# Optimization experiments

Hardware: AMD Instinct MI355X
Metric: run time of the kernel (lower is better)

Reference implementation:

```python
import jax, jax.numpy as jnp
import numpy as np

TEMPERATURE = 2.0
SOFT_LAMBDA = 0.5
SMOOTH_L1_BETA = 1.0  # CFG.smooth_l1_beta (torch default)
EPS_COS = 1e-8
EPS_LOG = 1e-7


def _offdiag(x):
    # x: [n, n] -> [n, n-1], dropping the diagonal, preserving column order.
    n = x.shape[0]
    cols = jnp.arange(n - 1)
    idx = cols[None, :] + (cols[None, :] >= jnp.arange(n)[:, None])
    return x[jnp.arange(n)[:, None], idx]


def _cos_pair_diff(v):
    # 1 - pairwise cosine similarity, norms clamped at eps (torch CosineSimilarity).
    nv = jnp.maximum(jnp.linalg.norm(v, axis=-1), EPS_COS)
    cos = (v @ v.T) / (nv[:, None] * nv[None, :])
    return 1.0 - cos


def setup_inputs() -> dict:
    key = jax.random.key(0)
    k1, k2, k3, k4, k5 = jax.random.split(key, 5)
    n, d_feat = 384, 128
    return {
        "trans_feat": jax.random.normal(k1, (n, d_feat), dtype=jnp.float32),
        "rot_green": jax.random.normal(k2, (n, 3), dtype=jnp.float32),
        "rot_red": jax.random.normal(k3, (n, 3), dtype=jnp.float32),
        "trans": jax.random.normal(k4, (n, 3), dtype=jnp.float32),
        "sym": jax.random.randint(k5, (n, 1), 0, 2, dtype=jnp.int32),
    }


def reference(trans_feat, rot_green, rot_red, trans, sym):
    n = trans_feat.shape[0]

    # ---- label differences ----
    # trans: smooth-L1 over pairwise diffs, mean over coord dim -> [n, n]
    d = trans[:, None, :] - trans[None, :, :]
    ad = jnp.abs(d)
    sl1 = jnp.where(ad < SMOOTH_L1_BETA, 0.5 * d * d / SMOOTH_L1_BETA, ad - 0.5 * SMOOTH_L1_BETA)
    trans_diff = sl1.mean(-1)

    g = _cos_pair_diff(rot_green)
    r = _cos_pair_diff(rot_red)
    sym_mask = sym[:, 0] == 1
    pair_sym = sym_mask[:, None] | sym_mask[None, :]
    rot_diff = jnp.where(pair_sym, g, g + r)

    # ---- feature similarity logits (negative L2, zero-safe norm) ----
    fd = trans_feat[:, None, :] - trans_feat[None, :, :]
    sq = jnp.sum(fd * fd, axis=-1)
    norm = jnp.where(sq > 0, jnp.sqrt(jnp.where(sq > 0, sq, 1.0)), 0.0)
    logits = -norm / TEMPERATURE
    logits = logits - jnp.max(logits, axis=1, keepdims=True)
    exp_logits = jnp.exp(logits)

    lo = _offdiag(logits)      # [n, n-1]
    eo = _offdiag(exp_logits)  # [n, n-1]
    td = _offdiag(trans_diff)  # [n, n-1]
    rd = _offdiag(rot_diff)    # [n, n-1]

    # rank masks: mask[i, j, k] = diff[i, j] <= diff[i, k]
    trans_mask = td[:, :, None] <= td[:, None, :]
    hard_mask = trans_mask & (rd[:, :, None] <= rd[:, None, :])

    den_trans = jnp.einsum('ijk,ik->ij', trans_mask.astype(lo.dtype), eo)
    den_hard = jnp.einsum('ijk,ik->ij', hard_mask.astype(lo.dtype), eo)

    pos_trans = lo - jnp.log(den_trans + EPS_LOG)
    pos_hard = lo - jnp.log(den_hard + EPS_LOG)

    denom = n * (n - 1)
    loss_hard = -jnp.sum(pos_hard) / denom
    loss_trans = -jnp.sum(pos_trans) / denom
    return loss_hard + SOFT_LAMBDA * loss_trans
```

## Files before the change

### kernel.cpp

```cpp
#include <hip/hip_runtime.h>
#include <math.h>

#define N 384
#define DF 128
#define TI 16
#define TK 16
#define TEMP 2.0f
#define SOFT_LAMBDA 0.5f
#define BETA 1.0f
#define EPS_COS 1e-8f
#define EPS_LOG 1e-7f

__global__ __launch_bounds__(256) void rnc_pairs(
    const float* __restrict__ feat,
    const float* __restrict__ rg,
    const float* __restrict__ rr,
    const float* __restrict__ tr,
    const int*   __restrict__ sym,
    float4* __restrict__ pk)
{
    const int i0 = blockIdx.y * TI;
    const int k0 = blockIdx.x * TK;
    const int t = threadIdx.x;

    __shared__ __align__(16) float4 fi_s[TI][DF / 4 + 1];
    __shared__ __align__(16) float4 fk_s[TK][DF / 4 + 1];
    __shared__ float4 hi_s[TI], gi_s[TI], ri_s[TI];
    __shared__ float4 hk_s[TK], gk_s[TK], rk_s[TK];

    if (t < TI) {
        int g = i0 + t;
        hi_s[t] = make_float4(tr[g * 3], tr[g * 3 + 1], tr[g * 3 + 2],
                              (sym[g] == 1) ? 1.f : 0.f);
        float a = rg[g * 3], b = rg[g * 3 + 1], c = rg[g * 3 + 2];
        gi_s[t] = make_float4(a, b, c, fmaxf(sqrtf(a * a + b * b + c * c), EPS_COS));
        float d = rr[g * 3], e = rr[g * 3 + 1], f = rr[g * 3 + 2];
        ri_s[t] = make_float4(d, e, f, fmaxf(sqrtf(d * d + e * e + f * f), EPS_COS));
    } else if (t >= 32 && t < 32 + TK) {
        int g = k0 + (t - 32);
        int tl = t - 32;
        hk_s[tl] = make_float4(tr[g * 3], tr[g * 3 + 1], tr[g * 3 + 2],
                               (sym[g] == 1) ? 1.f : 0.f);
        float a = rg[g * 3], b = rg[g * 3 + 1], c = rg[g * 3 + 2];
        gk_s[tl] = make_float4(a, b, c, fmaxf(sqrtf(a * a + b * b + c * c), EPS_COS));
        float d = rr[g * 3], e = rr[g * 3 + 1], f = rr[g * 3 + 2];
        rk_s[tl] = make_float4(d, e, f, fmaxf(sqrtf(d * d + e * e + f * f), EPS_COS));
    }

    const float4* feat4 = reinterpret_cast<const float4*>(feat);
#pragma unroll
    for (int idx = 0; idx < 2; ++idx) {
        int u = t + idx * 256;
        int row = u >> 5, c = u & 31;
        fi_s[row][c] = feat4[(i0 + row) * (DF / 4) + c];
        fk_s[row][c] = feat4[(k0 + row) * (DF / 4) + c];
    }
    __syncthreads();

    const int ii = t >> 4, kk = t & 15;
    float sq = 0.f;
#pragma unroll
    for (int d = 0; d < DF / 4; ++d) {
        float4 a = fi_s[ii][d];
        float4 b = fk_s[kk][d];
        float dx = a.x - b.x, dy = a.y - b.y, dz = a.z - b.z, dw = a.w - b.w;
        sq += dx * dx + dy * dy + dz * dz + dw * dw;
    }
    const int gi = i0 + ii, gk = k0 + kk;
    float dist = (sq > 0.f) ? sqrtf(sq) : 0.f;
    float lo = -dist * (1.0f / TEMP);
    float eo = (gi == gk) ? 0.f : expf(lo);

    float4 ha = hi_s[ii], hb = hk_s[kk];
    float s = 0.f;
    {
        float d0 = ha.x - hb.x, d1 = ha.y - hb.y, d2 = ha.z - hb.z;
        float a0 = fabsf(d0), a1 = fabsf(d1), a2 = fabsf(d2);
        s += (a0 < BETA) ? (0.5f * d0 * d0 / BETA) : (a0 - 0.5f * BETA);
        s += (a1 < BETA) ? (0.5f * d1 * d1 / BETA) : (a1 - 0.5f * BETA);
        s += (a2 < BETA) ? (0.5f * d2 * d2 / BETA) : (a2 - 0.5f * BETA);
    }
    float td = s * (1.0f / 3.0f);

    float4 ga = gi_s[ii], gb = gk_s[kk];
    float gdiff = 1.0f - (ga.x * gb.x + ga.y * gb.y + ga.z * gb.z) / (ga.w * gb.w);
    float4 ra = ri_s[ii], rb = rk_s[kk];
    float rdiff = 1.0f - (ra.x * rb.x + ra.y * rb.y + ra.z * rb.z) / (ra.w * rb.w);
    bool pair_sym = (ha.w != 0.f) || (hb.w != 0.f);
    float rd = pair_sym ? gdiff : (gdiff + rdiff);

    pk[gi * N + gk] = make_float4(td, rd, eo, lo);
}

__global__ __launch_bounds__(512) void rnc_rank(
    const float4* __restrict__ pk,
    float* __restrict__ partial_h,
    float* __restrict__ partial_t)
{
    const int i = blockIdx.x >> 1;
    const int h = blockIdx.x & 1;
    const int t = threadIdx.x;

    __shared__ __align__(16) float4 pks[N];
    __shared__ __align__(16) float2 dp[192][8];
    __shared__ float red_h[8], red_t[8];

    if (t < N) pks[t] = pk[i * N + t];
    __syncthreads();

    const int w = t >> 6, l = t & 63;
    const int jl = l * 3;
    float tdj[3], rdj[3];
    float dent[3] = {0.f, 0.f, 0.f};
    float denh[3] = {0.f, 0.f, 0.f};
#pragma unroll
    for (int jj = 0; jj < 3; ++jj) {
        float4 p = pks[h * 192 + jl + jj];
        tdj[jj] = p.x;
        rdj[jj] = p.y;
    }
    const int k0 = w * 48;
#pragma unroll 4
    for (int k = k0; k < k0 + 48; ++k) {
        float4 p = pks[k];
#pragma unroll
        for (int jj = 0; jj < 3; ++jj) {
            bool mt = p.x >= tdj[jj];
            bool mh = mt && (p.y >= rdj[jj]);
            dent[jj] += mt ? p.z : 0.f;
            denh[jj] += mh ? p.z : 0.f;
        }
    }
#pragma unroll
    for (int jj = 0; jj < 3; ++jj) dp[jl + jj][w] = make_float2(dent[jj], denh[jj]);
    __syncthreads();

    float pos_h = 0.f, pos_t = 0.f;
    if (t < 192) {
        const int j = h * 192 + t;
        if (j != i) {
            float st_ = 0.f, sh_ = 0.f;
#pragma unroll
            for (int g = 0; g < 8; ++g) {
                float2 v = dp[t][g];
                st_ += v.x;
                sh_ += v.y;
            }
            float lo = pks[j].w;
            pos_h = lo - logf(sh_ + EPS_LOG);
            pos_t = lo - logf(st_ + EPS_LOG);
        }
    }
#pragma unroll
    for (int off = 32; off > 0; off >>= 1) {
        pos_h += __shfl_down(pos_h, off, 64);
        pos_t += __shfl_down(pos_t, off, 64);
    }
    if (l == 0) {
        red_h[w] = pos_h;
        red_t[w] = pos_t;
    }
    __syncthreads();
    if (t == 0) {
        float sh = 0.f, st = 0.f;
#pragma unroll
        for (int g = 0; g < 8; ++g) {
            sh += red_h[g];
            st += red_t[g];
        }
        partial_h[blockIdx.x] = sh;
        partial_t[blockIdx.x] = st;
    }
}

__global__ __launch_bounds__(768) void rnc_final(
    const float* __restrict__ partial_h,
    const float* __restrict__ partial_t,
    float* __restrict__ out)
{
    const int t = threadIdx.x;
    float hsum = partial_h[t];
    float tsum = partial_t[t];
#pragma unroll
    for (int off = 32; off > 0; off >>= 1) {
        hsum += __shfl_down(hsum, off, 64);
        tsum += __shfl_down(tsum, off, 64);
    }
    __shared__ float rh[12], rt[12];
    const int wave = t >> 6, lane = t & 63;
    if (lane == 0) {
        rh[wave] = hsum;
        rt[wave] = tsum;
    }
    __syncthreads();
    if (t == 0) {
        double sh = 0.0, st = 0.0;
#pragma unroll
        for (int w = 0; w < 12; ++w) {
            sh += (double)rh[w];
            st += (double)rt[w];
        }
        const double denom = (double)N * (double)(N - 1);
        out[0] = (float)(-(sh + (double)SOFT_LAMBDA * st) / denom);
    }
}

extern "C" void kernel_launch(void* const* d_in, const int* in_sizes, int n_in,
                              void* d_out, int out_size, void* d_ws, size_t ws_size,
                              hipStream_t stream) {
    const float* feat = (const float*)d_in[0];
    const float* rg   = (const float*)d_in[1];
    const float* rr   = (const float*)d_in[2];
    const float* tr   = (const float*)d_in[3];
    const int*   sym  = (const int*)d_in[4];
    float* out = (float*)d_out;

    float4* pk = (float4*)d_ws;
    float* partial_h = (float*)((char*)d_ws + (size_t)N * N * sizeof(float4));
    float* partial_t = partial_h + 2 * N;

    dim3 gridA(N / TK, N / TI);
    rnc_pairs<<<gridA, 256, 0, stream>>>(feat, rg, rr, tr, sym, pk);
    rnc_rank<<<2 * N, 512, 0, stream>>>(pk, partial_h, partial_t);
    rnc_final<<<1, 2 * N, 0, stream>>>(partial_h, partial_t, out);
}
```

Baseline: 79.81 us.

## Use norm-expansion dot products with 2x2 register tiles and atomic final reduce

The pairwise feature kernel now computes squared distances as |a|^2+|b|^2-2a·b, using 64-thread blocks where each thread produces a 2x2 tile of pairs so shared-memory loads are reused. The third reduction kernel is removed: the rank kernel atomically adds its scaled partial sums into the output, which the first kernel zeroes. This cuts one launch and reduces the LDS traffic per pair. In exchange it adds cancellation error in the distance and a nondeterministic float atomic summation order.

```diff
diff --git a/kernel.cpp b/kernel.cpp
--- a/kernel.cpp
+++ b/kernel.cpp
@@ -3,32 +3,41 @@
 
 #define N 384
 #define DF 128
-#define TI 16
-#define TK 16
 #define TEMP 2.0f
 #define SOFT_LAMBDA 0.5f
 #define BETA 1.0f
 #define EPS_COS 1e-8f
 #define EPS_LOG 1e-7f
 
-__global__ __launch_bounds__(256) void rnc_pairs(
+__global__ __launch_bounds__(64) void rnc_pairs(
     const float* __restrict__ feat,
     const float* __restrict__ rg,
     const float* __restrict__ rr,
     const float* __restrict__ tr,
     const int*   __restrict__ sym,
-    float4* __restrict__ pk)
+    float4* __restrict__ pk,
+    float* __restrict__ out)
 {
-    const int i0 = blockIdx.y * TI;
-    const int k0 = blockIdx.x * TK;
+    const int i0 = blockIdx.y * 16;
+    const int k0 = blockIdx.x * 16;
     const int t = threadIdx.x;
 
-    __shared__ __align__(16) float4 fi_s[TI][DF / 4 + 1];
-    __shared__ __align__(16) float4 fk_s[TK][DF / 4 + 1];
-    __shared__ float4 hi_s[TI], gi_s[TI], ri_s[TI];
-    __shared__ float4 hk_s[TK], gk_s[TK], rk_s[TK];
-
-    if (t < TI) {
+    __shared__ __align__(16) float4 fa[16][33];
+    __shared__ __align__(16) float4 fb[16][33];
+    __shared__ float nsq[2][16];
+    __shared__ float4 hi_s[16], gi_s[16], ri_s[16];
+    __shared__ float4 hk_s[16], gk_s[16], rk_s[16];
+
+    if (blockIdx.x == 0 && blockIdx.y == 0 && t == 0) out[0] = 0.f;
+
+    const float4* feat4 = reinterpret_cast<const float4*>(feat);
+#pragma unroll
+    for (int u = t; u < 512; u += 64) {
+        int row = u >> 5, c = u & 31;
+        fa[row][c] = feat4[(i0 + row) * (DF / 4) + c];
+        fb[row][c] = feat4[(k0 + row) * (DF / 4) + c];
+    }
+    if (t < 16) {
         int g = i0 + t;
         hi_s[t] = make_float4(tr[g * 3], tr[g * 3 + 1], tr[g * 3 + 2],
                               (sym[g] == 1) ? 1.f : 0.f);
@@ -36,9 +45,8 @@
         gi_s[t] = make_float4(a, b, c, fmaxf(sqrtf(a * a + b * b + c * c), EPS_COS));
         float d = rr[g * 3], e = rr[g * 3 + 1], f = rr[g * 3 + 2];
         ri_s[t] = make_float4(d, e, f, fmaxf(sqrtf(d * d + e * e + f * f), EPS_COS));
-    } else if (t >= 32 && t < 32 + TK) {
-        int g = k0 + (t - 32);
-        int tl = t - 32;
+    } else if (t < 32) {
+        int tl = t - 16, g = k0 + tl;
         hk_s[tl] = make_float4(tr[g * 3], tr[g * 3 + 1], tr[g * 3 + 2],
                                (sym[g] == 1) ? 1.f : 0.f);
         float a = rg[g * 3], b = rg[g * 3 + 1], c = rg[g * 3 + 2];
@@ -46,56 +54,70 @@
         float d = rr[g * 3], e = rr[g * 3 + 1], f = rr[g * 3 + 2];
         rk_s[tl] = make_float4(d, e, f, fmaxf(sqrtf(d * d + e * e + f * f), EPS_COS));
     }
-
-    const float4* feat4 = reinterpret_cast<const float4*>(feat);
-#pragma unroll
-    for (int idx = 0; idx < 2; ++idx) {
-        int u = t + idx * 256;
-        int row = u >> 5, c = u & 31;
-        fi_s[row][c] = feat4[(i0 + row) * (DF / 4) + c];
-        fk_s[row][c] = feat4[(k0 + row) * (DF / 4) + c];
-    }
-    __syncthreads();
-
-    const int ii = t >> 4, kk = t & 15;
-    float sq = 0.f;
-#pragma unroll
-    for (int d = 0; d < DF / 4; ++d) {
-        float4 a = fi_s[ii][d];
-        float4 b = fk_s[kk][d];
-        float dx = a.x - b.x, dy = a.y - b.y, dz = a.z - b.z, dw = a.w - b.w;
-        sq += dx * dx + dy * dy + dz * dz + dw * dw;
-    }
-    const int gi = i0 + ii, gk = k0 + kk;
-    float dist = (sq > 0.f) ? sqrtf(sq) : 0.f;
-    float lo = -dist * (1.0f / TEMP);
-    float eo = (gi == gk) ? 0.f : expf(lo);
-
-    float4 ha = hi_s[ii], hb = hk_s[kk];
-    float s = 0.f;
-    {
-        float d0 = ha.x - hb.x, d1 = ha.y - hb.y, d2 = ha.z - hb.z;
-        float a0 = fabsf(d0), a1 = fabsf(d1), a2 = fabsf(d2);
-        s += (a0 < BETA) ? (0.5f * d0 * d0 / BETA) : (a0 - 0.5f * BETA);
-        s += (a1 < BETA) ? (0.5f * d1 * d1 / BETA) : (a1 - 0.5f * BETA);
-        s += (a2 < BETA) ? (0.5f * d2 * d2 / BETA) : (a2 - 0.5f * BETA);
-    }
-    float td = s * (1.0f / 3.0f);
-
-    float4 ga = gi_s[ii], gb = gk_s[kk];
-    float gdiff = 1.0f - (ga.x * gb.x + ga.y * gb.y + ga.z * gb.z) / (ga.w * gb.w);
-    float4 ra = ri_s[ii], rb = rk_s[kk];
-    float rdiff = 1.0f - (ra.x * rb.x + ra.y * rb.y + ra.z * rb.z) / (ra.w * rb.w);
-    bool pair_sym = (ha.w != 0.f) || (hb.w != 0.f);
-    float rd = pair_sym ? gdiff : (gdiff + rdiff);
-
-    pk[gi * N + gk] = make_float4(td, rd, eo, lo);
+    __syncthreads();
+
+    if (t < 32) {
+        int which = t >> 4, r = t & 15;
+        float s = 0.f;
+#pragma unroll
+        for (int d4 = 0; d4 < DF / 4; ++d4) {
+            float4 v = which ? fb[r][d4] : fa[r][d4];
+            s += v.x * v.x + v.y * v.y + v.z * v.z + v.w * v.w;
+        }
+        nsq[which][r] = s;
+    }
+    __syncthreads();
+
+    const int tx = t & 7, ty = t >> 3;
+    const int ia = 2 * ty, ka = 2 * tx;
+    float d00 = 0.f, d01 = 0.f, d10 = 0.f, d11 = 0.f;
+#pragma unroll
+    for (int d4 = 0; d4 < DF / 4; ++d4) {
+        float4 a0 = fa[ia][d4];
+        float4 a1 = fa[ia + 1][d4];
+        float4 b0 = fb[ka][d4];
+        float4 b1 = fb[ka + 1][d4];
+        d00 += a0.x * b0.x + a0.y * b0.y + a0.z * b0.z + a0.w * b0.w;
+        d01 += a0.x * b1.x + a0.y * b1.y + a0.z * b1.z + a0.w * b1.w;
+        d10 += a1.x * b0.x + a1.y * b0.y + a1.z * b0.z + a1.w * b0.w;
+        d11 += a1.x * b1.x + a1.y * b1.y + a1.z * b1.z + a1.w * b1.w;
+    }
+    float dots[2][2] = {{d00, d01}, {d10, d11}};
+
+#pragma unroll
+    for (int ii = 0; ii < 2; ++ii) {
+#pragma unroll
+        for (int kk = 0; kk < 2; ++kk) {
+            const int li = ia + ii, lk = ka + kk;
+            const int gi = i0 + li, gk = k0 + lk;
+            float sq = nsq[0][li] + nsq[1][lk] - 2.f * dots[ii][kk];
+            float dist = (sq > 0.f) ? sqrtf(sq) : 0.f;
+            float lo = -dist * (1.0f / TEMP);
+            float eo = (gi == gk) ? 0.f : expf(lo);
+
+            float4 ha = hi_s[li], hb = hk_s[lk];
+            float d0 = ha.x - hb.x, d1 = ha.y - hb.y, d2 = ha.z - hb.z;
+            float a0 = fabsf(d0), a1 = fabsf(d1), a2 = fabsf(d2);
+            float s = ((a0 < BETA) ? (0.5f * d0 * d0 / BETA) : (a0 - 0.5f * BETA))
+                    + ((a1 < BETA) ? (0.5f * d1 * d1 / BETA) : (a1 - 0.5f * BETA))
+                    + ((a2 < BETA) ? (0.5f * d2 * d2 / BETA) : (a2 - 0.5f * BETA));
+            float td = s * (1.0f / 3.0f);
+
+            float4 ga = gi_s[li], gb = gk_s[lk];
+            float gdiff = 1.0f - (ga.x * gb.x + ga.y * gb.y + ga.z * gb.z) / (ga.w * gb.w);
+            float4 ra = ri_s[li], rb = rk_s[lk];
+            float rdiff = 1.0f - (ra.x * rb.x + ra.y * rb.y + ra.z * rb.z) / (ra.w * rb.w);
+            bool pair_sym = (ha.w != 0.f) || (hb.w != 0.f);
+            float rd = pair_sym ? gdiff : (gdiff + rdiff);
+
+            pk[gi * N + gk] = make_float4(td, rd, eo, lo);
+        }
+    }
 }
 
 __global__ __launch_bounds__(512) void rnc_rank(
     const float4* __restrict__ pk,
-    float* __restrict__ partial_h,
-    float* __restrict__ partial_t)
+    float* __restrict__ out)
 {
     const int i = blockIdx.x >> 1;
     const int h = blockIdx.x & 1;
@@ -168,40 +190,8 @@
             sh += red_h[g];
             st += red_t[g];
         }
-        partial_h[blockIdx.x] = sh;
-        partial_t[blockIdx.x] = st;
-    }
-}
-
-__global__ __launch_bounds__(768) void rnc_final(
-    const float* __restrict__ partial_h,
-    const float* __restrict__ partial_t,
-    float* __restrict__ out)
-{
-    const int t = threadIdx.x;
-    float hsum = partial_h[t];
-    float tsum = partial_t[t];
-#pragma unroll
-    for (int off = 32; off > 0; off >>= 1) {
-        hsum += __shfl_down(hsum, off, 64);
-        tsum += __shfl_down(tsum, off, 64);
-    }
-    __shared__ float rh[12], rt[12];
-    const int wave = t >> 6, lane = t & 63;
-    if (lane == 0) {
-        rh[wave] = hsum;
-        rt[wave] = tsum;
-    }
-    __syncthreads();
-    if (t == 0) {
-        double sh = 0.0, st = 0.0;
-#pragma unroll
-        for (int w = 0; w < 12; ++w) {
-            sh += (double)rh[w];
-            st += (double)rt[w];
-        }
-        const double denom = (double)N * (double)(N - 1);
-        out[0] = (float)(-(sh + (double)SOFT_LAMBDA * st) / denom);
+        const float scale = -1.0f / ((float)N * (float)(N - 1));
+        atomicAdd(out, (sh + SOFT_LAMBDA * st) * scale);
     }
 }
 
@@ -216,11 +206,8 @@
     float* out = (float*)d_out;
 
     float4* pk = (float4*)d_ws;
-    float* partial_h = (float*)((char*)d_ws + (size_t)N * N * sizeof(float4));
-    float* partial_t = partial_h + 2 * N;
-
-    dim3 gridA(N / TK, N / TI);
-    rnc_pairs<<<gridA, 256, 0, stream>>>(feat, rg, rr, tr, sym, pk);
-    rnc_rank<<<2 * N, 512, 0, stream>>>(pk, partial_h, partial_t);
-    rnc_final<<<1, 2 * N, 0, stream>>>(partial_h, partial_t, out);
+
+    dim3 gridA(N / 16, N / 16);
+    rnc_pairs<<<gridA, 64, 0, stream>>>(feat, rg, rr, tr, sym, pk, out);
+    rnc_rank<<<2 * N, 512, 0, stream>>>(pk, out);
 }
```

Result: slower. 84.58 us (+6.0%).

## Drop final reduction kernel via atomicAdd and process full rows per rank block

Applied to the files above, without the earlier changes.

The separate final-reduction launch is removed. The pairs kernel zeroes the output, and each rank block atomically adds its scaled partial sum into it. The rank kernel now handles a whole row i per block, six j per thread instead of three, which halves the block count and reloads each pk row once instead of twice. This saves one launch and the duplicated row loads, at the cost of more register pressure, fewer blocks for parallelism, and non-deterministic float atomic accumulation order.

```diff
diff --git a/kernel.cpp b/kernel.cpp
--- a/kernel.cpp
+++ b/kernel.cpp
@@ -17,7 +17,8 @@
     const float* __restrict__ rr,
     const float* __restrict__ tr,
     const int*   __restrict__ sym,
-    float4* __restrict__ pk)
+    float4* __restrict__ pk,
+    float* __restrict__ out)
 {
     const int i0 = blockIdx.y * TI;
     const int k0 = blockIdx.x * TK;
@@ -27,6 +28,8 @@
     __shared__ __align__(16) float4 fk_s[TK][DF / 4 + 1];
     __shared__ float4 hi_s[TI], gi_s[TI], ri_s[TI];
     __shared__ float4 hk_s[TK], gk_s[TK], rk_s[TK];
+
+    if (blockIdx.x == 0 && blockIdx.y == 0 && t == 0) out[0] = 0.f;
 
     if (t < TI) {
         int g = i0 + t;
@@ -72,14 +75,11 @@
     float eo = (gi == gk) ? 0.f : expf(lo);
 
     float4 ha = hi_s[ii], hb = hk_s[kk];
-    float s = 0.f;
-    {
-        float d0 = ha.x - hb.x, d1 = ha.y - hb.y, d2 = ha.z - hb.z;
-        float a0 = fabsf(d0), a1 = fabsf(d1), a2 = fabsf(d2);
-        s += (a0 < BETA) ? (0.5f * d0 * d0 / BETA) : (a0 - 0.5f * BETA);
-        s += (a1 < BETA) ? (0.5f * d1 * d1 / BETA) : (a1 - 0.5f * BETA);
-        s += (a2 < BETA) ? (0.5f * d2 * d2 / BETA) : (a2 - 0.5f * BETA);
-    }
+    float d0 = ha.x - hb.x, d1 = ha.y - hb.y, d2 = ha.z - hb.z;
+    float a0 = fabsf(d0), a1 = fabsf(d1), a2 = fabsf(d2);
+    float s = ((a0 < BETA) ? (0.5f * d0 * d0 / BETA) : (a0 - 0.5f * BETA))
+            + ((a1 < BETA) ? (0.5f * d1 * d1 / BETA) : (a1 - 0.5f * BETA))
+            + ((a2 < BETA) ? (0.5f * d2 * d2 / BETA) : (a2 - 0.5f * BETA));
     float td = s * (1.0f / 3.0f);
 
     float4 ga = gi_s[ii], gb = gk_s[kk];
@@ -94,28 +94,27 @@
 
 __global__ __launch_bounds__(512) void rnc_rank(
     const float4* __restrict__ pk,
-    float* __restrict__ partial_h,
-    float* __restrict__ partial_t)
+    float* __restrict__ out)
 {
-    const int i = blockIdx.x >> 1;
-    const int h = blockIdx.x & 1;
+    const int i = blockIdx.x;
     const int t = threadIdx.x;
 
     __shared__ __align__(16) float4 pks[N];
-    __shared__ __align__(16) float2 dp[192][8];
+    __shared__ float dpt[8][N];
+    __shared__ float dph[8][N];
     __shared__ float red_h[8], red_t[8];
 
     if (t < N) pks[t] = pk[i * N + t];
     __syncthreads();
 
     const int w = t >> 6, l = t & 63;
-    const int jl = l * 3;
-    float tdj[3], rdj[3];
-    float dent[3] = {0.f, 0.f, 0.f};
-    float denh[3] = {0.f, 0.f, 0.f};
+    const int jb = l * 6;
+    float tdj[6], rdj[6];
+    float dent[6] = {0.f, 0.f, 0.f, 0.f, 0.f, 0.f};
+    float denh[6] = {0.f, 0.f, 0.f, 0.f, 0.f, 0.f};
 #pragma unroll
-    for (int jj = 0; jj < 3; ++jj) {
-        float4 p = pks[h * 192 + jl + jj];
+    for (int jj = 0; jj < 6; ++jj) {
+        float4 p = pks[jb + jj];
         tdj[jj] = p.x;
         rdj[jj] = p.y;
     }
@@ -124,7 +123,7 @@
     for (int k = k0; k < k0 + 48; ++k) {
         float4 p = pks[k];
 #pragma unroll
-        for (int jj = 0; jj < 3; ++jj) {
+        for (int jj = 0; jj < 6; ++jj) {
             bool mt = p.x >= tdj[jj];
             bool mh = mt && (p.y >= rdj[jj]);
             dent[jj] += mt ? p.z : 0.f;
@@ -132,24 +131,23 @@
         }
     }
 #pragma unroll
-    for (int jj = 0; jj < 3; ++jj) dp[jl + jj][w] = make_float2(dent[jj], denh[jj]);
+    for (int jj = 0; jj < 6; ++jj) {
+        dpt[w][jb + jj] = dent[jj];
+        dph[w][jb + jj] = denh[jj];
+    }
     __syncthreads();
 
     float pos_h = 0.f, pos_t = 0.f;
-    if (t < 192) {
-        const int j = h * 192 + t;
-        if (j != i) {
-            float st_ = 0.f, sh_ = 0.f;
+    if (t < N && t != i) {
+        float st_ = 0.f, sh_ = 0.f;
 #pragma unroll
-            for (int g = 0; g < 8; ++g) {
-                float2 v = dp[t][g];
-                st_ += v.x;
-                sh_ += v.y;
-            }
-            float lo = pks[j].w;
-            pos_h = lo - logf(sh_ + EPS_LOG);
-            pos_t = lo - logf(st_ + EPS_LOG);
+        for (int g = 0; g < 8; ++g) {
+            st_ += dpt[g][t];
+            sh_ += dph[g][t];
         }
+        float lo = pks[t].w;
+        pos_h = lo - logf(sh_ + EPS_LOG);
+        pos_t = lo - logf(st_ + EPS_LOG);
     }
 #pragma unroll
     for (int off = 32; off > 0; off >>= 1) {
@@ -168,40 +166,8 @@
             sh += red_h[g];
             st += red_t[g];
         }
-        partial_h[blockIdx.x] = sh;
-        partial_t[blockIdx.x] = st;
-    }
-}
-
-__global__ __launch_bounds__(768) void rnc_final(
-    const float* __restrict__ partial_h,
-    const float* __restrict__ partial_t,
-    float* __restrict__ out)
-{
-    const int t = threadIdx.x;
-    float hsum = partial_h[t];
-    float tsum = partial_t[t];
-#pragma unroll
-    for (int off = 32; off > 0; off >>= 1) {
-        hsum += __shfl_down(hsum, off, 64);
-        tsum += __shfl_down(tsum, off, 64);
-    }
-    __shared__ float rh[12], rt[12];
-    const int wave = t >> 6, lane = t & 63;
-    if (lane == 0) {
-        rh[wave] = hsum;
-        rt[wave] = tsum;
-    }
-    __syncthreads();
-    if (t == 0) {
-        double sh = 0.0, st = 0.0;
-#pragma unroll
-        for (int w = 0; w < 12; ++w) {
-            sh += (double)rh[w];
-            st += (double)rt[w];
-        }
-        const double denom = (double)N * (double)(N - 1);
-        out[0] = (float)(-(sh + (double)SOFT_LAMBDA * st) / denom);
+        const float scale = -1.0f / ((float)N * (float)(N - 1));
+        atomicAdd(out, (sh + SOFT_LAMBDA * st) * scale);
     }
 }
 
@@ -216,11 +182,8 @@
     float* out = (float*)d_out;
 
     float4* pk = (float4*)d_ws;
-    float* partial_h = (float*)((char*)d_ws + (size_t)N * N * sizeof(float4));
-    float* partial_t = partial_h + 2 * N;
 
     dim3 gridA(N / TK, N / TI);
-    rnc_pairs<<<gridA, 256, 0, stream>>>(feat, rg, rr, tr, sym, pk);
-    rnc_rank<<<2 * N, 512, 0, stream>>>(pk, partial_h, partial_t);
-    rnc_final<<<1, 2 * N, 0, stream>>>(partial_h, partial_t, out);
+    rnc_pairs<<<gridA, 256, 0, stream>>>(feat, rg, rr, tr, sym, pk, out);
+    rnc_rank<<<N, 512, 0, stream>>>(pk, out);
 }
```

After: 81.67 us. 2.3% more time.
